# Performance work log

Measured on AMD Instinct MI355X. Metric: run time of the kernel, lower is better.

Reference implementation:

```python
import jax, jax.numpy as jnp
import numpy as np

N = 50000
NEG_SLOPE = 0.2
BN_EPS = 1e-5


def _self_loops(src, dst, n):
    loop = jnp.arange(n, dtype=src.dtype)
    return jnp.concatenate([src, loop]), jnp.concatenate([dst, loop])


def gcn_conv(x, src, dst, W, b, n):
    # PyG GCNConv: add self-loops, symmetric deg^-1/2 normalization, scatter-add.
    h = x @ W                                             # [N, C]
    s, d = _self_loops(src, dst, n)
    deg = jax.ops.segment_sum(jnp.ones_like(d, dtype=h.dtype), d, num_segments=n)
    dinv = jnp.where(deg > 0, jax.lax.rsqrt(deg), 0.0)
    norm = dinv[s] * dinv[d]                              # [E+N]
    out = jax.ops.segment_sum(h[s] * norm[:, None], d, num_segments=n)
    return out + b


def gat_conv(x, src, dst, W, a_src, a_dst, b, n, heads):
    # PyG GATConv (concat=False, eval mode: no dropout): add self-loops,
    # per-edge LeakyReLU attention logits, segment-softmax over dst, mean heads.
    C = W.shape[1] // heads
    h = (x @ W).reshape(n, heads, C)                      # [N, H, C]
    s, d = _self_loops(src, dst, n)
    al_s = jnp.sum(h * a_src[None], axis=-1)              # [N, H]
    al_d = jnp.sum(h * a_dst[None], axis=-1)              # [N, H]
    e = jax.nn.leaky_relu(al_s[s] + al_d[d], NEG_SLOPE)   # [E+N, H]
    emax = jax.ops.segment_max(e, d, num_segments=n)[d]
    ex = jnp.exp(e - emax)
    denom = jax.ops.segment_sum(ex, d, num_segments=n)[d]
    alpha = ex / denom                                    # [E+N, H]
    out = jax.ops.segment_sum(h[s] * alpha[:, :, None], d, num_segments=n)
    return jnp.mean(out, axis=1) + b                      # concat=False -> head mean


def batch_norm(x, g, b, m, v):
    # eval-mode BatchNorm1d with running stats
    return (x - m) * jax.lax.rsqrt(v + BN_EPS) * g + b


def setup_inputs() -> dict:
    key = jax.random.key(0)
    ks = jax.random.split(key, 12)
    E = 800000
    inp = {}
    inp['x'] = jax.random.normal(ks[0], (N, 128), dtype=jnp.float32)
    inp['edge_index'] = jax.random.randint(ks[1], (2, E), 0, N, dtype=jnp.int64)
    inp['gcn1_W'] = jax.random.normal(ks[2], (128, 96), dtype=jnp.float32) * 0.08
    inp['gcn1_b'] = jnp.zeros((96,), jnp.float32)
    inp['bn1_g'] = jnp.ones((96,), jnp.float32)
    inp['bn1_b'] = jnp.zeros((96,), jnp.float32)
    inp['bn1_m'] = jnp.zeros((96,), jnp.float32)
    inp['bn1_v'] = jnp.ones((96,), jnp.float32)
    inp['gat1_W'] = jax.random.normal(ks[3], (96, 192), dtype=jnp.float32) * 0.1
    inp['gat1_as'] = jax.random.normal(ks[4], (2, 96), dtype=jnp.float32) * 0.1
    inp['gat1_ad'] = jax.random.normal(ks[5], (2, 96), dtype=jnp.float32) * 0.1
    inp['gat1_b'] = jnp.zeros((96,), jnp.float32)
    inp['gcn2_W'] = jax.random.normal(ks[6], (96, 96), dtype=jnp.float32) * 0.1
    inp['gcn2_b'] = jnp.zeros((96,), jnp.float32)
    inp['bn2_g'] = jnp.ones((96,), jnp.float32)
    inp['bn2_b'] = jnp.zeros((96,), jnp.float32)
    inp['bn2_m'] = jnp.zeros((96,), jnp.float32)
    inp['bn2_v'] = jnp.ones((96,), jnp.float32)
    inp['gat2_W'] = jax.random.normal(ks[7], (96, 80), dtype=jnp.float32) * 0.1
    inp['gat2_as'] = jax.random.normal(ks[8], (2, 40), dtype=jnp.float32) * 0.1
    inp['gat2_ad'] = jax.random.normal(ks[9], (2, 40), dtype=jnp.float32) * 0.1
    inp['gat2_b'] = jnp.zeros((40,), jnp.float32)
    return inp


def reference(x, edge_index, gcn1_W, gcn1_b, bn1_g, bn1_b, bn1_m, bn1_v,
              gat1_W, gat1_as, gat1_ad, gat1_b, gcn2_W, gcn2_b,
              bn2_g, bn2_b, bn2_m, bn2_v, gat2_W, gat2_as, gat2_ad, gat2_b):
    src, dst = edge_index[0], edge_index[1]
    h = gcn_conv(x, src, dst, gcn1_W, gcn1_b, N)
    h = jax.nn.relu(batch_norm(h, bn1_g, bn1_b, bn1_m, bn1_v))
    h = jax.nn.relu(gat_conv(h, src, dst, gat1_W, gat1_as, gat1_ad, gat1_b, N, 2))
    h = gcn_conv(h, src, dst, gcn2_W, gcn2_b, N)
    h = jax.nn.relu(batch_norm(h, bn2_g, bn2_b, bn2_m, bn2_v))
    h = gat_conv(h, src, dst, gat2_W, gat2_as, gat2_ad, gat2_b, N, 2)
    return jax.nn.log_softmax(h, axis=1)
```

## Files before the change

### kernel.cpp

```cpp
#include <hip/hip_runtime.h>
#include <math.h>

#define NNODES 50000
#define NEG_SLOPE 0.2f
#define BN_EPS 1e-5f

typedef __attribute__((ext_vector_type(8))) short bf16x8;
typedef __attribute__((ext_vector_type(4))) float f32x4;

static __device__ __forceinline__ float leaky(float x) {
    return x > 0.f ? x : NEG_SLOPE * x;
}
static __device__ __forceinline__ unsigned short f2bf(float x) {
    unsigned u = __float_as_uint(x);
    u += 0x7FFFu + ((u >> 16) & 1u);
    return (unsigned short)(u >> 16);
}
static __device__ __forceinline__ void unpack8(uint4 u, float* v) {
    v[0] = __uint_as_float(u.x << 16);
    v[1] = __uint_as_float(u.x & 0xFFFF0000u);
    v[2] = __uint_as_float(u.y << 16);
    v[3] = __uint_as_float(u.y & 0xFFFF0000u);
    v[4] = __uint_as_float(u.z << 16);
    v[5] = __uint_as_float(u.z & 0xFFFF0000u);
    v[6] = __uint_as_float(u.w << 16);
    v[7] = __uint_as_float(u.w & 0xFFFF0000u);
}
static __device__ __forceinline__ void acc8(uint4 u, float w, float* a) {
    float v[8]; unpack8(u, v);
#pragma unroll
    for (int j = 0; j < 8; ++j) a[j] = fmaf(w, v[j], a[j]);
}
static __device__ __forceinline__ uint4 pack8(const float* o) {
    uint4 r;
    r.x = ((unsigned)f2bf(o[1]) << 16) | f2bf(o[0]);
    r.y = ((unsigned)f2bf(o[3]) << 16) | f2bf(o[2]);
    r.z = ((unsigned)f2bf(o[5]) << 16) | f2bf(o[4]);
    r.w = ((unsigned)f2bf(o[7]) << 16) | f2bf(o[6]);
    return r;
}

__global__ void k_zero_deg(int* degi, int n) {
    int v = blockIdx.x * blockDim.x + threadIdx.x;
    if (v < n) degi[v] = 0;
}
__global__ void k_count(const int* __restrict__ dst, int* degi, int E) {
    int e = blockIdx.x * blockDim.x + threadIdx.x;
    if (e < E) atomicAdd(&degi[dst[e]], 1);
}
__global__ void k_scan1(const int* __restrict__ degi, int* __restrict__ incl,
                        int* __restrict__ bsum, int n) {
    __shared__ int s[256];
    int i = blockIdx.x * 256 + threadIdx.x;
    int v = (i < n) ? degi[i] : 0;
    s[threadIdx.x] = v;
    __syncthreads();
    for (int off = 1; off < 256; off <<= 1) {
        int t = (threadIdx.x >= (unsigned)off) ? s[threadIdx.x - off] : 0;
        __syncthreads();
        s[threadIdx.x] += t;
        __syncthreads();
    }
    if (i < n) incl[i] = s[threadIdx.x];
    if (threadIdx.x == 255) bsum[blockIdx.x] = s[255];
}
__global__ void k_scan2(int* bsum, int nb) {
    __shared__ int s[256];
    int v = ((int)threadIdx.x < nb) ? bsum[threadIdx.x] : 0;
    s[threadIdx.x] = v;
    __syncthreads();
    for (int off = 1; off < 256; off <<= 1) {
        int t = (threadIdx.x >= (unsigned)off) ? s[threadIdx.x - off] : 0;
        __syncthreads();
        s[threadIdx.x] += t;
        __syncthreads();
    }
    if ((int)threadIdx.x < nb) bsum[threadIdx.x] = s[threadIdx.x];
}
__global__ void k_scan3(const int* __restrict__ degi, const int* __restrict__ incl,
                        const int* __restrict__ bsum, int* __restrict__ row_ptr,
                        int* __restrict__ cursor, float* __restrict__ dinv, int n) {
    int i = blockIdx.x * 256 + threadIdx.x;
    if (i >= n) return;
    int off = (blockIdx.x > 0) ? bsum[blockIdx.x - 1] : 0;
    int inc = incl[i] + off;
    row_ptr[i + 1] = inc;
    cursor[i] = inc - degi[i];
    dinv[i] = rsqrtf((float)(degi[i] + 1));
    if (i == 0) row_ptr[0] = 0;
}
__global__ void k_fill(const int* __restrict__ src, const int* __restrict__ dst,
                       int* cursor, int* __restrict__ csr_src, int E) {
    int e = blockIdx.x * blockDim.x + threadIdx.x;
    if (e >= E) return;
    int pos = atomicAdd(&cursor[dst[e]], 1);
    csr_src[pos] = src[e];
}

__global__ void k_wconv(const float* __restrict__ W, unsigned short* __restrict__ out,
                        int Ki, int Ko) {
    int idx = blockIdx.x * blockDim.x + threadIdx.x;
    if (idx >= Ki * Ko) return;
    int k = idx / Ko, c = idx % Ko;
    out[c * Ki + k] = f2bf(W[idx]);
}
__global__ void k_xconv(const float4* __restrict__ x, uint4* __restrict__ out, int n8) {
    int i = blockIdx.x * blockDim.x + threadIdx.x;
    if (i >= n8) return;
    float4 a = x[i * 2], b = x[i * 2 + 1];
    float o[8] = {a.x, a.y, a.z, a.w, b.x, b.y, b.z, b.w};
    out[i] = pack8(o);
}

template<int KI, int KO>
__launch_bounds__(256)
__global__ void k_gemm_mfma(const unsigned short* __restrict__ A,
                            const unsigned short* __restrict__ WT,
                            unsigned short* __restrict__ C, int n) {
    constexpr int KP = KI + 8;
    constexpr int NT = KO / 16;
    constexpr int KT = KI / 32;
    __shared__ unsigned short wT[KO][KP];
    const int t = threadIdx.x;
    const int w = t >> 6, l = t & 63;

    constexpr int CH = KI / 8;
    for (int idx = t; idx < KO * CH; idx += 256) {
        int r = idx / CH, o = idx % CH;
        *(uint4*)&wT[r][o * 8] = *(const uint4*)&WT[r * KI + o * 8];
    }
    int row = blockIdx.x * 64 + w * 16 + (l & 15);
    bool rv = row < n;
    const unsigned short* ap = A + (long long)row * KI + (l >> 4) * 8;
    bf16x8 afr[KT];
#pragma unroll
    for (int kt = 0; kt < KT; ++kt) {
        bf16x8 z = {};
        afr[kt] = rv ? *(const bf16x8*)(ap + kt * 32) : z;
    }
    __syncthreads();

    f32x4 acc[NT];
#pragma unroll
    for (int ct = 0; ct < NT; ++ct) acc[ct] = (f32x4){0.f, 0.f, 0.f, 0.f};
#pragma unroll
    for (int kt = 0; kt < KT; ++kt) {
#pragma unroll
        for (int ct = 0; ct < NT; ++ct) {
            bf16x8 b = *(const bf16x8*)&wT[ct * 16 + (l & 15)][kt * 32 + (l >> 4) * 8];
            acc[ct] = __builtin_amdgcn_mfma_f32_16x16x32_bf16(afr[kt], b, acc[ct], 0, 0, 0);
        }
    }
    int orow0 = blockIdx.x * 64 + w * 16 + (l >> 4) * 4;
    int col = l & 15;
#pragma unroll
    for (int ct = 0; ct < NT; ++ct) {
#pragma unroll
        for (int r = 0; r < 4; ++r) {
            int rr = orow0 + r;
            if (rr < n) C[(long long)rr * KO + ct * 16 + col] = f2bf(acc[ct][r]);
        }
    }
}

__global__ void k_gcn_gather_bn8(const uint4* __restrict__ hb, const int* __restrict__ row_ptr,
                                 const int* __restrict__ csr_src, const float* __restrict__ dinv,
                                 const float* __restrict__ bias, const float* __restrict__ g,
                                 const float* __restrict__ b, const float* __restrict__ m,
                                 const float* __restrict__ vv,
                                 uint4* __restrict__ outb, int n, int Q8) {
    int t = blockIdx.x * blockDim.x + threadIdx.x;
    if (t >= n * Q8) return;
    int v = t / Q8, q = t % Q8;
    int beg = row_ptr[v], end = row_ptr[v + 1];
    float dv = dinv[v];
    float a[8] = {0.f, 0.f, 0.f, 0.f, 0.f, 0.f, 0.f, 0.f};
    acc8(hb[(long long)v * Q8 + q], dv, a);
    int p = beg;
    for (; p + 2 <= end; p += 2) {
        int s0 = csr_src[p], s1 = csr_src[p + 1];
        float w0 = dinv[s0], w1 = dinv[s1];
        uint4 u0 = hb[(long long)s0 * Q8 + q];
        uint4 u1 = hb[(long long)s1 * Q8 + q];
        acc8(u0, w0, a);
        acc8(u1, w1, a);
    }
    if (p < end) {
        int s = csr_src[p];
        acc8(hb[(long long)s * Q8 + q], dinv[s], a);
    }
    int c0 = q * 8;
    float o[8];
#pragma unroll
    for (int j = 0; j < 8; ++j) {
        int c = c0 + j;
        float x = fmaf(a[j], dv, bias[c]);
        x = (x - m[c]) * rsqrtf(vv[c] + BN_EPS) * g[c] + b[c];
        o[j] = fmaxf(x, 0.f);
    }
    outb[(long long)v * Q8 + q] = pack8(o);
}

__global__ void k_gat_logits8(const uint4* __restrict__ hb, const float* __restrict__ as,
                              const float* __restrict__ ad, float* __restrict__ alS,
                              float* __restrict__ alD, int n, int C) {
    int t = blockIdx.x * blockDim.x + threadIdx.x;
    if (t >= n * 2) return;
    int hh = t & 1;
    int C8 = C >> 3;
    const uint4* row = hb + (long long)t * C8;
    float s1 = 0.f, s2 = 0.f;
    for (int q = 0; q < C8; ++q) {
        float v[8]; unpack8(row[q], v);
#pragma unroll
        for (int j = 0; j < 8; ++j) {
            int c = hh * C + q * 8 + j;
            s1 = fmaf(v[j], as[c], s1);
            s2 = fmaf(v[j], ad[c], s2);
        }
    }
    alS[t] = s1; alD[t] = s2;
}
__global__ void k_gat_vh(const int* __restrict__ row_ptr, const int* __restrict__ csr_src,
                         const float* __restrict__ alS, const float* __restrict__ alD,
                         float* __restrict__ eex, float* __restrict__ selfw,
                         float* __restrict__ invden, int n, int H) {
    int t = blockIdx.x * blockDim.x + threadIdx.x;
    if (t >= n * H) return;
    int v = t / H, h = t % H;
    int beg = row_ptr[v], end = row_ptr[v + 1];
    float ad = alD[t];
    float l_self = leaky(alS[t] + ad);
    float mx = l_self;
    int p = beg;
    for (; p + 2 <= end; p += 2) {
        int s0 = csr_src[p], s1 = csr_src[p + 1];
        float l0 = leaky(alS[s0 * H + h] + ad);
        float l1 = leaky(alS[s1 * H + h] + ad);
        eex[p * H + h] = l0;
        eex[(p + 1) * H + h] = l1;
        mx = fmaxf(mx, fmaxf(l0, l1));
    }
    if (p < end) {
        int s = csr_src[p];
        float l = leaky(alS[s * H + h] + ad);
        eex[p * H + h] = l;
        mx = fmaxf(mx, l);
    }
    float exs = expf(l_self - mx);
    float den = exs;
    p = beg;
    for (; p + 2 <= end; p += 2) {
        float e0 = expf(eex[p * H + h] - mx);
        float e1 = expf(eex[(p + 1) * H + h] - mx);
        eex[p * H + h] = e0;
        eex[(p + 1) * H + h] = e1;
        den += e0 + e1;
    }
    if (p < end) {
        float e = expf(eex[p * H + h] - mx);
        eex[p * H + h] = e;
        den += e;
    }
    selfw[t] = exs;
    invden[t] = 1.f / den;
}
template<int OUTBF>
__global__ void k_gat_gather2_8(const uint4* __restrict__ hb, const int* __restrict__ row_ptr,
                                const int* __restrict__ csr_src, const float2* __restrict__ eex2,
                                const float2* __restrict__ selfw2, const float2* __restrict__ invden2,
                                const float* __restrict__ bias, uint4* __restrict__ outb,
                                float4* __restrict__ outf, int n, int Q8, int do_relu) {
    int t = blockIdx.x * blockDim.x + threadIdx.x;
    if (t >= n * Q8) return;
    int v = t / Q8, q = t % Q8;
    int rowOct = 2 * Q8;
    int beg = row_ptr[v], end = row_ptr[v + 1];
    float A0[8] = {0,0,0,0,0,0,0,0}, A1[8] = {0,0,0,0,0,0,0,0};
    {
        float2 sw = selfw2[v];
        const uint4* hv = hb + (long long)v * rowOct;
        acc8(hv[q], sw.x, A0);
        acc8(hv[Q8 + q], sw.y, A1);
    }
    int p = beg;
    for (; p + 2 <= end; p += 2) {
        int s0 = csr_src[p], s1 = csr_src[p + 1];
        float2 w0 = eex2[p], w1 = eex2[p + 1];
        const uint4* h0 = hb + (long long)s0 * rowOct;
        const uint4* h1 = hb + (long long)s1 * rowOct;
        uint4 u00 = h0[q], u01 = h0[Q8 + q];
        uint4 u10 = h1[q], u11 = h1[Q8 + q];
        acc8(u00, w0.x, A0);
        acc8(u01, w0.y, A1);
        acc8(u10, w1.x, A0);
        acc8(u11, w1.y, A1);
    }
    if (p < end) {
        int s = csr_src[p];
        float2 w = eex2[p];
        const uint4* hs = hb + (long long)s * rowOct;
        acc8(hs[q], w.x, A0);
        acc8(hs[Q8 + q], w.y, A1);
    }
    float2 idn = invden2[v];
    int c0 = q * 8;
    float o[8];
#pragma unroll
    for (int j = 0; j < 8; ++j) {
        float x = fmaf(0.5f, fmaf(A0[j], idn.x, A1[j] * idn.y), bias[c0 + j]);
        o[j] = do_relu ? fmaxf(x, 0.f) : x;
    }
    if (OUTBF) {
        outb[(long long)v * Q8 + q] = pack8(o);
    } else {
        long long ob = (long long)v * (Q8 * 2) + q * 2;
        outf[ob]     = make_float4(o[0], o[1], o[2], o[3]);
        outf[ob + 1] = make_float4(o[4], o[5], o[6], o[7]);
    }
}

__global__ void k_logsoftmax40(const float* __restrict__ in, float* __restrict__ out, int n) {
    int v = blockIdx.x * blockDim.x + threadIdx.x;
    if (v >= n) return;
    float vals[40];
    float mx = -INFINITY;
#pragma unroll
    for (int c = 0; c < 40; ++c) {
        float x = in[v * 40 + c];
        vals[c] = x;
        mx = fmaxf(mx, x);
    }
    float s = 0.f;
#pragma unroll
    for (int c = 0; c < 40; ++c) s += expf(vals[c] - mx);
    float ls = logf(s);
#pragma unroll
    for (int c = 0; c < 40; ++c) out[v * 40 + c] = vals[c] - mx - ls;
}

static inline int nblk(long long n, int b) { return (int)((n + b - 1) / b); }

extern "C" void kernel_launch(void* const* d_in, const int* in_sizes, int n_in,
                              void* d_out, int out_size, void* d_ws, size_t ws_size,
                              hipStream_t stream) {
    const float* x       = (const float*)d_in[0];
    const int*   ei      = (const int*)d_in[1];
    const float* gcn1_W  = (const float*)d_in[2];
    const float* gcn1_b  = (const float*)d_in[3];
    const float* bn1_g   = (const float*)d_in[4];
    const float* bn1_b   = (const float*)d_in[5];
    const float* bn1_m   = (const float*)d_in[6];
    const float* bn1_v   = (const float*)d_in[7];
    const float* gat1_W  = (const float*)d_in[8];
    const float* gat1_as = (const float*)d_in[9];
    const float* gat1_ad = (const float*)d_in[10];
    const float* gat1_b  = (const float*)d_in[11];
    const float* gcn2_W  = (const float*)d_in[12];
    const float* gcn2_b  = (const float*)d_in[13];
    const float* bn2_g   = (const float*)d_in[14];
    const float* bn2_b   = (const float*)d_in[15];
    const float* bn2_m   = (const float*)d_in[16];
    const float* bn2_v   = (const float*)d_in[17];
    const float* gat2_W  = (const float*)d_in[18];
    const float* gat2_as = (const float*)d_in[19];
    const float* gat2_ad = (const float*)d_in[20];
    const float* gat2_b  = (const float*)d_in[21];

    const int n = NNODES;
    const int E = in_sizes[1] / 2;
    const int* src = ei;
    const int* dst = ei + E;

    char* p = (char*)d_ws;
    float* dinv    = (float*)p; p += 50048 * 4;
    int*   degi    = (int*)p;   p += 50048 * 4;
    int*   row_ptr = (int*)p;   p += 50052 * 4;
    int*   cursor  = (int*)p;   p += 50048 * 4;
    int*   incl    = (int*)p;   p += 50048 * 4;
    int*   bsum    = (int*)p;   p += 256 * 4;
    int*   csr_src = (int*)p;   p += 800000 * 4;
    unsigned short* hbf = (unsigned short*)p; p += 9600000 * 2;
    unsigned short* abf = (unsigned short*)p; p += 6400000 * 2;
    unsigned short* wbf = (unsigned short*)p; p += 47616 * 2 + 64;
    float* bufA    = (float*)p; p += 2000000 * 4;
    float* alS     = (float*)p; p += 100096 * 4;
    float* alD     = (float*)p; p += 100096 * 4;
    float* selfw   = (float*)p; p += 100096 * 4;
    float* invden  = (float*)p; p += 100096 * 4;
    float* eex     = (float*)p; p += 1600000 * 4;

    unsigned short* w1T = wbf;
    unsigned short* w2T = wbf + 12288;
    unsigned short* w3T = wbf + 12288 + 18432;
    unsigned short* w4T = wbf + 12288 + 18432 + 9216;

    const int B = 256;
    const int GB = nblk(n, 64);
    const int SB = nblk(n, 256);
    float* out = (float*)d_out;

    k_wconv<<<nblk(128 * 96, B), B, 0, stream>>>(gcn1_W, w1T, 128, 96);
    k_wconv<<<nblk(96 * 192, B), B, 0, stream>>>(gat1_W, w2T, 96, 192);
    k_wconv<<<nblk(96 * 96, B), B, 0, stream>>>(gcn2_W, w3T, 96, 96);
    k_wconv<<<nblk(96 * 80, B), B, 0, stream>>>(gat2_W, w4T, 96, 80);
    k_xconv<<<nblk((long long)n * 16, B), B, 0, stream>>>((const float4*)x, (uint4*)abf, n * 16);

    k_zero_deg<<<nblk(n, B), B, 0, stream>>>(degi, n);
    k_count<<<nblk(E, B), B, 0, stream>>>(dst, degi, E);
    k_scan1<<<SB, 256, 0, stream>>>(degi, incl, bsum, n);
    k_scan2<<<1, 256, 0, stream>>>(bsum, SB);
    k_scan3<<<SB, 256, 0, stream>>>(degi, incl, bsum, row_ptr, cursor, dinv, n);
    k_fill<<<nblk(E, B), B, 0, stream>>>(src, dst, cursor, csr_src, E);

    k_gemm_mfma<128, 96><<<GB, 256, 0, stream>>>(abf, w1T, hbf, n);
    k_gcn_gather_bn8<<<nblk((long long)n * 12, B), B, 0, stream>>>(
        (const uint4*)hbf, row_ptr, csr_src, dinv, gcn1_b, bn1_g, bn1_b, bn1_m, bn1_v,
        (uint4*)abf, n, 12);

    k_gemm_mfma<96, 192><<<GB, 256, 0, stream>>>(abf, w2T, hbf, n);
    k_gat_logits8<<<nblk(n * 2, B), B, 0, stream>>>((const uint4*)hbf, gat1_as, gat1_ad, alS, alD, n, 96);
    k_gat_vh<<<nblk(n * 2, B), B, 0, stream>>>(row_ptr, csr_src, alS, alD, eex, selfw, invden, n, 2);
    k_gat_gather2_8<1><<<nblk((long long)n * 12, B), B, 0, stream>>>(
        (const uint4*)hbf, row_ptr, csr_src, (const float2*)eex, (const float2*)selfw,
        (const float2*)invden, gat1_b, (uint4*)abf, nullptr, n, 12, 1);

    k_gemm_mfma<96, 96><<<GB, 256, 0, stream>>>(abf, w3T, hbf, n);
    k_gcn_gather_bn8<<<nblk((long long)n * 12, B), B, 0, stream>>>(
        (const uint4*)hbf, row_ptr, csr_src, dinv, gcn2_b, bn2_g, bn2_b, bn2_m, bn2_v,
        (uint4*)abf, n, 12);

    k_gemm_mfma<96, 80><<<GB, 256, 0, stream>>>(abf, w4T, hbf, n);
    k_gat_logits8<<<nblk(n * 2, B), B, 0, stream>>>((const uint4*)hbf, gat2_as, gat2_ad, alS, alD, n, 40);
    k_gat_vh<<<nblk(n * 2, B), B, 0, stream>>>(row_ptr, csr_src, alS, alD, eex, selfw, invden, n, 2);
    k_gat_gather2_8<0><<<nblk((long long)n * 5, B), B, 0, stream>>>(
        (const uint4*)hbf, row_ptr, csr_src, (const float2*)eex, (const float2*)selfw,
        (const float2*)invden, gat2_b, nullptr, (float4*)bufA, n, 5, 0);

    k_logsoftmax40<<<nblk(n, B), B, 0, stream>>>(bufA, out, n);
}
```

Measured before the change: 385.5 us.

## Use online softmax for GAT, recompute exp in gather, unroll gathers by four

Result: slower. 422.5 us (+9.6%).

```diff
diff --git a/kernel.cpp b/kernel.cpp
--- a/kernel.cpp
+++ b/kernel.cpp
@@ -40,10 +40,6 @@
     return r;
 }
 
-__global__ void k_zero_deg(int* degi, int n) {
-    int v = blockIdx.x * blockDim.x + threadIdx.x;
-    if (v < n) degi[v] = 0;
-}
 __global__ void k_count(const int* __restrict__ dst, int* degi, int E) {
     int e = blockIdx.x * blockDim.x + threadIdx.x;
     if (e < E) atomicAdd(&degi[dst[e]], 1);
@@ -163,6 +159,7 @@
     }
 }
 
+__launch_bounds__(256, 8)
 __global__ void k_gcn_gather_bn8(const uint4* __restrict__ hb, const int* __restrict__ row_ptr,
                                  const int* __restrict__ csr_src, const float* __restrict__ dinv,
                                  const float* __restrict__ bias, const float* __restrict__ g,
@@ -177,15 +174,19 @@
     float a[8] = {0.f, 0.f, 0.f, 0.f, 0.f, 0.f, 0.f, 0.f};
     acc8(hb[(long long)v * Q8 + q], dv, a);
     int p = beg;
-    for (; p + 2 <= end; p += 2) {
-        int s0 = csr_src[p], s1 = csr_src[p + 1];
-        float w0 = dinv[s0], w1 = dinv[s1];
+    for (; p + 4 <= end; p += 4) {
+        int s0 = csr_src[p], s1 = csr_src[p + 1], s2 = csr_src[p + 2], s3 = csr_src[p + 3];
+        float w0 = dinv[s0], w1 = dinv[s1], w2 = dinv[s2], w3 = dinv[s3];
         uint4 u0 = hb[(long long)s0 * Q8 + q];
         uint4 u1 = hb[(long long)s1 * Q8 + q];
+        uint4 u2 = hb[(long long)s2 * Q8 + q];
+        uint4 u3 = hb[(long long)s3 * Q8 + q];
         acc8(u0, w0, a);
         acc8(u1, w1, a);
-    }
-    if (p < end) {
+        acc8(u2, w2, a);
+        acc8(u3, w3, a);
+    }
+    for (; p < end; ++p) {
         int s = csr_src[p];
         acc8(hb[(long long)s * Q8 + q], dinv[s], a);
     }
@@ -221,54 +222,52 @@
     }
     alS[t] = s1; alD[t] = s2;
 }
-__global__ void k_gat_vh(const int* __restrict__ row_ptr, const int* __restrict__ csr_src,
-                         const float* __restrict__ alS, const float* __restrict__ alD,
-                         float* __restrict__ eex, float* __restrict__ selfw,
-                         float* __restrict__ invden, int n, int H) {
-    int t = blockIdx.x * blockDim.x + threadIdx.x;
-    if (t >= n * H) return;
-    int v = t / H, h = t % H;
+__global__ void k_gat_vh2(const int* __restrict__ row_ptr, const int* __restrict__ csr_src,
+                          const float2* __restrict__ alS2, const float2* __restrict__ alD2,
+                          float2* __restrict__ eex2, float2* __restrict__ selfa2,
+                          float2* __restrict__ off2, int n) {
+    int v = blockIdx.x * blockDim.x + threadIdx.x;
+    if (v >= n) return;
     int beg = row_ptr[v], end = row_ptr[v + 1];
-    float ad = alD[t];
-    float l_self = leaky(alS[t] + ad);
-    float mx = l_self;
+    float2 ad = alD2[v], as0 = alS2[v];
+    float ls0 = leaky(as0.x + ad.x), ls1 = leaky(as0.y + ad.y);
+    float m0 = ls0, m1 = ls1, d0 = 1.f, d1 = 1.f;
     int p = beg;
     for (; p + 2 <= end; p += 2) {
         int s0 = csr_src[p], s1 = csr_src[p + 1];
-        float l0 = leaky(alS[s0 * H + h] + ad);
-        float l1 = leaky(alS[s1 * H + h] + ad);
-        eex[p * H + h] = l0;
-        eex[(p + 1) * H + h] = l1;
-        mx = fmaxf(mx, fmaxf(l0, l1));
+        float2 a0 = alS2[s0], a1 = alS2[s1];
+        float l00 = leaky(a0.x + ad.x), l01 = leaky(a0.y + ad.y);
+        float l10 = leaky(a1.x + ad.x), l11 = leaky(a1.y + ad.y);
+        eex2[p] = make_float2(l00, l01);
+        eex2[p + 1] = make_float2(l10, l11);
+        float nm0 = fmaxf(m0, fmaxf(l00, l10));
+        d0 = d0 * expf(m0 - nm0) + expf(l00 - nm0) + expf(l10 - nm0);
+        m0 = nm0;
+        float nm1 = fmaxf(m1, fmaxf(l01, l11));
+        d1 = d1 * expf(m1 - nm1) + expf(l01 - nm1) + expf(l11 - nm1);
+        m1 = nm1;
     }
     if (p < end) {
         int s = csr_src[p];
-        float l = leaky(alS[s * H + h] + ad);
-        eex[p * H + h] = l;
-        mx = fmaxf(mx, l);
-    }
-    float exs = expf(l_self - mx);
-    float den = exs;
-    p = beg;
-    for (; p + 2 <= end; p += 2) {
-        float e0 = expf(eex[p * H + h] - mx);
-        float e1 = expf(eex[(p + 1) * H + h] - mx);
-        eex[p * H + h] = e0;
-        eex[(p + 1) * H + h] = e1;
-        den += e0 + e1;
-    }
-    if (p < end) {
-        float e = expf(eex[p * H + h] - mx);
-        eex[p * H + h] = e;
-        den += e;
-    }
-    selfw[t] = exs;
-    invden[t] = 1.f / den;
+        float2 a = alS2[s];
+        float l0 = leaky(a.x + ad.x), l1 = leaky(a.y + ad.y);
+        eex2[p] = make_float2(l0, l1);
+        float nm0 = fmaxf(m0, l0);
+        d0 = d0 * expf(m0 - nm0) + expf(l0 - nm0);
+        m0 = nm0;
+        float nm1 = fmaxf(m1, l1);
+        d1 = d1 * expf(m1 - nm1) + expf(l1 - nm1);
+        m1 = nm1;
+    }
+    float o0 = m0 + logf(d0), o1 = m1 + logf(d1);
+    off2[v] = make_float2(o0, o1);
+    selfa2[v] = make_float2(expf(ls0 - o0), expf(ls1 - o1));
 }
 template<int OUTBF>
+__launch_bounds__(256, 6)
 __global__ void k_gat_gather2_8(const uint4* __restrict__ hb, const int* __restrict__ row_ptr,
                                 const int* __restrict__ csr_src, const float2* __restrict__ eex2,
-                                const float2* __restrict__ selfw2, const float2* __restrict__ invden2,
+                                const float2* __restrict__ selfa2, const float2* __restrict__ off2,
                                 const float* __restrict__ bias, uint4* __restrict__ outb,
                                 float4* __restrict__ outf, int n, int Q8, int do_relu) {
     int t = blockIdx.x * blockDim.x + threadIdx.x;
@@ -276,39 +275,48 @@
     int v = t / Q8, q = t % Q8;
     int rowOct = 2 * Q8;
     int beg = row_ptr[v], end = row_ptr[v + 1];
+    float2 off = off2[v];
     float A0[8] = {0,0,0,0,0,0,0,0}, A1[8] = {0,0,0,0,0,0,0,0};
     {
-        float2 sw = selfw2[v];
+        float2 sa = selfa2[v];
         const uint4* hv = hb + (long long)v * rowOct;
-        acc8(hv[q], sw.x, A0);
-        acc8(hv[Q8 + q], sw.y, A1);
+        acc8(hv[q], sa.x, A0);
+        acc8(hv[Q8 + q], sa.y, A1);
     }
     int p = beg;
-    for (; p + 2 <= end; p += 2) {
-        int s0 = csr_src[p], s1 = csr_src[p + 1];
-        float2 w0 = eex2[p], w1 = eex2[p + 1];
+    for (; p + 4 <= end; p += 4) {
+        int s0 = csr_src[p], s1 = csr_src[p + 1], s2 = csr_src[p + 2], s3 = csr_src[p + 3];
+        float2 l0 = eex2[p], l1 = eex2[p + 1], l2 = eex2[p + 2], l3 = eex2[p + 3];
         const uint4* h0 = hb + (long long)s0 * rowOct;
         const uint4* h1 = hb + (long long)s1 * rowOct;
+        const uint4* h2 = hb + (long long)s2 * rowOct;
+        const uint4* h3 = hb + (long long)s3 * rowOct;
         uint4 u00 = h0[q], u01 = h0[Q8 + q];
         uint4 u10 = h1[q], u11 = h1[Q8 + q];
-        acc8(u00, w0.x, A0);
-        acc8(u01, w0.y, A1);
-        acc8(u10, w1.x, A0);
-        acc8(u11, w1.y, A1);
-    }
-    if (p < end) {
+        uint4 u20 = h2[q], u21 = h2[Q8 + q];
+        uint4 u30 = h3[q], u31 = h3[Q8 + q];
+        float a00 = expf(l0.x - off.x), a01 = expf(l0.y - off.y);
+        float a10 = expf(l1.x - off.x), a11 = expf(l1.y - off.y);
+        float a20 = expf(l2.x - off.x), a21 = expf(l2.y - off.y);
+        float a30 = expf(l3.x - off.x), a31 = expf(l3.y - off.y);
+        acc8(u00, a00, A0); acc8(u01, a01, A1);
+        acc8(u10, a10, A0); acc8(u11, a11, A1);
+        acc8(u20, a20, A0); acc8(u21, a21, A1);
+        acc8(u30, a30, A0); acc8(u31, a31, A1);
+    }
+    for (; p < end; ++p) {
         int s = csr_src[p];
-        float2 w = eex2[p];
+        float2 l = eex2[p];
         const uint4* hs = hb + (long long)s * rowOct;
-        acc8(hs[q], w.x, A0);
-        acc8(hs[Q8 + q], w.y, A1);
-    }
-    float2 idn = invden2[v];
+        float a0 = expf(l.x - off.x), a1 = expf(l.y - off.y);
+        acc8(hs[q], a0, A0);
+        acc8(hs[Q8 + q], a1, A1);
+    }
     int c0 = q * 8;
     float o[8];
 #pragma unroll
     for (int j = 0; j < 8; ++j) {
-        float x = fmaf(0.5f, fmaf(A0[j], idn.x, A1[j] * idn.y), bias[c0 + j]);
+        float x = fmaf(0.5f, A0[j] + A1[j], bias[c0 + j]);
         o[j] = do_relu ? fmaxf(x, 0.f) : x;
     }
     if (OUTBF) {
@@ -386,8 +394,8 @@
     float* bufA    = (float*)p; p += 2000000 * 4;
     float* alS     = (float*)p; p += 100096 * 4;
     float* alD     = (float*)p; p += 100096 * 4;
-    float* selfw   = (float*)p; p += 100096 * 4;
-    float* invden  = (float*)p; p += 100096 * 4;
+    float* selfa   = (float*)p; p += 100096 * 4;
+    float* offv    = (float*)p; p += 100096 * 4;
     float* eex     = (float*)p; p += 1600000 * 4;
 
     unsigned short* w1T = wbf;
@@ -406,7 +414,7 @@
     k_wconv<<<nblk(96 * 80, B), B, 0, stream>>>(gat2_W, w4T, 96, 80);
     k_xconv<<<nblk((long long)n * 16, B), B, 0, stream>>>((const float4*)x, (uint4*)abf, n * 16);
 
-    k_zero_deg<<<nblk(n, B), B, 0, stream>>>(degi, n);
+    hipMemsetAsync(degi, 0, (size_t)n * 4, stream);
     k_count<<<nblk(E, B), B, 0, stream>>>(dst, degi, E);
     k_scan1<<<SB, 256, 0, stream>>>(degi, incl, bsum, n);
     k_scan2<<<1, 256, 0, stream>>>(bsum, SB);
@@ -420,10 +428,11 @@
 
     k_gemm_mfma<96, 192><<<GB, 256, 0, stream>>>(abf, w2T, hbf, n);
     k_gat_logits8<<<nblk(n * 2, B), B, 0, stream>>>((const uint4*)hbf, gat1_as, gat1_ad, alS, alD, n, 96);
-    k_gat_vh<<<nblk(n * 2, B), B, 0, stream>>>(row_ptr, csr_src, alS, alD, eex, selfw, invden, n, 2);
+    k_gat_vh2<<<nblk(n, B), B, 0, stream>>>(row_ptr, csr_src, (const float2*)alS, (const float2*)alD,
+                                            (float2*)eex, (float2*)selfa, (float2*)offv, n);
     k_gat_gather2_8<1><<<nblk((long long)n * 12, B), B, 0, stream>>>(
-        (const uint4*)hbf, row_ptr, csr_src, (const float2*)eex, (const float2*)selfw,
-        (const float2*)invden, gat1_b, (uint4*)abf, nullptr, n, 12, 1);
+        (const uint4*)hbf, row_ptr, csr_src, (const float2*)eex, (const float2*)selfa,
+        (const float2*)offv, gat1_b, (uint4*)abf, nullptr, n, 12, 1);
 
     k_gemm_mfma<96, 96><<<GB, 256, 0, stream>>>(abf, w3T, hbf, n);
     k_gcn_gather_bn8<<<nblk((long long)n * 12, B), B, 0, stream>>>(
@@ -432,10 +441,11 @@
 
     k_gemm_mfma<96, 80><<<GB, 256, 0, stream>>>(abf, w4T, hbf, n);
     k_gat_logits8<<<nblk(n * 2, B), B, 0, stream>>>((const uint4*)hbf, gat2_as, gat2_ad, alS, alD, n, 40);
-    k_gat_vh<<<nblk(n * 2, B), B, 0, stream>>>(row_ptr, csr_src, alS, alD, eex, selfw, invden, n, 2);
+    k_gat_vh2<<<nblk(n, B), B, 0, stream>>>(row_ptr, csr_src, (const float2*)alS, (const float2*)alD,
+                                            (float2*)eex, (float2*)selfa, (float2*)offv, n);
     k_gat_gather2_8<0><<<nblk((long long)n * 5, B), B, 0, stream>>>(
-        (const uint4*)hbf, row_ptr, csr_src, (const float2*)eex, (const float2*)selfw,
-        (const float2*)invden, gat2_b, nullptr, (float4*)bufA, n, 5, 0);
+        (const uint4*)hbf, row_ptr, csr_src, (const float2*)eex, (const float2*)selfa,
+        (const float2*)offv, gat2_b, nullptr, (float4*)bufA, n, 5, 0);
 
     k_logsoftmax40<<<nblk(n, B), B, 0, stream>>>(bufA, out, n);
 }
```
